# Performance work log

Measured on AMD Instinct MI355X. Metric: run time of the kernel, lower is better.

Reference implementation:

```python
import jax, jax.numpy as jnp
import numpy as np

N = 100000
E = 1600000
FEAT = 128
EMBED = 128
CLASSES = 40


def _sage_conv(x, src, dst, W_l, W_r, b, n_nodes):
    # PyG SAGEConv (mean aggr): out = mean_{j in N(i)} x_j @ W_l + x_i @ W_r + b
    msg = x[src]                                                  # [E, d] gather
    agg = jax.ops.segment_sum(msg, dst, num_segments=n_nodes)     # [N, d]
    cnt = jax.ops.segment_sum(jnp.ones((src.shape[0], 1), x.dtype), dst,
                              num_segments=n_nodes)               # [N, 1]
    agg = agg / jnp.maximum(cnt, 1.0)                             # mean (0 for isolated)
    return agg @ W_l + x @ W_r + b


def setup_inputs() -> dict:
    key = jax.random.key(0)
    ks = jax.random.split(key, 10)
    s = lambda d: 1.0 / np.sqrt(d)
    x = jax.random.normal(ks[0], (N, FEAT), dtype=jnp.float32)
    edge_index = jax.random.randint(ks[1], (2, E), 0, N, dtype=jnp.int64)
    W1_l = jax.random.uniform(ks[2], (FEAT, EMBED), jnp.float32, -s(FEAT), s(FEAT))
    W1_r = jax.random.uniform(ks[3], (FEAT, EMBED), jnp.float32, -s(FEAT), s(FEAT))
    b1 = jnp.zeros((EMBED,), jnp.float32)
    W2_l = jax.random.uniform(ks[4], (EMBED, EMBED), jnp.float32, -s(EMBED), s(EMBED))
    W2_r = jax.random.uniform(ks[5], (EMBED, EMBED), jnp.float32, -s(EMBED), s(EMBED))
    b2 = jnp.zeros((EMBED,), jnp.float32)
    W_out = jax.random.uniform(ks[6], (EMBED, CLASSES), jnp.float32, -s(EMBED), s(EMBED))
    b_out = jax.random.uniform(ks[7], (CLASSES,), jnp.float32, -s(EMBED), s(EMBED))
    return {"x": x, "edge_index": edge_index,
            "W1_l": W1_l, "W1_r": W1_r, "b1": b1,
            "W2_l": W2_l, "W2_r": W2_r, "b2": b2,
            "W_out": W_out, "b_out": b_out}


def reference(x, edge_index, W1_l, W1_r, b1, W2_l, W2_r, b2, W_out, b_out):
    src, dst = edge_index[0], edge_index[1]
    n = x.shape[0]
    h = _sage_conv(x, src, dst, W1_l, W1_r, b1, n)   # [N, EMBED]
    h = _sage_conv(h, src, dst, W2_l, W2_r, b2, n)   # [N, EMBED]
    g = jnp.mean(h, axis=0, keepdims=True)           # global_mean_pool, batch=None -> [1, EMBED]
    return g @ W_out + b_out                          # [1, CLASSES]
```

## Files before the change

kernel.cpp:

```cpp
#include <hip/hip_runtime.h>


#define NN    100000
#define NE    1600000
#define NE4   (NE/4)
#define FEAT  128
#define NCLS  40
#define FSB   2048

#define RSC   12500
#define NRC   8
#define NCC   32
#define PERC  12500

#define RSV   16000
#define NRV   7
#define NCV   32
#define PERV  12500


__global__ __launch_bounds__(1024) void k_cnt(const int4* __restrict__ dst4,
                                              unsigned* __restrict__ pc) {
    __shared__ unsigned tab[RSC / 2];
    const int c = blockIdx.x, r = blockIdx.y;
    for (int j = threadIdx.x; j < RSC / 2; j += 1024) tab[j] = 0u;
    __syncthreads();
    const int base = r * RSC;
    const int i0 = c * PERC;
    for (int i = i0 + (int)threadIdx.x; i < i0 + PERC; i += 1024) {
        int4 d = dst4[i];
        unsigned a;
        a = (unsigned)(d.x - base); if (a < RSC) atomicAdd(&tab[a >> 1], 1u << ((a & 1) * 16));
        a = (unsigned)(d.y - base); if (a < RSC) atomicAdd(&tab[a >> 1], 1u << ((a & 1) * 16));
        a = (unsigned)(d.z - base); if (a < RSC) atomicAdd(&tab[a >> 1], 1u << ((a & 1) * 16));
        a = (unsigned)(d.w - base); if (a < RSC) atomicAdd(&tab[a >> 1], 1u << ((a & 1) * 16));
    }
    __syncthreads();
    unsigned* outp = pc + (size_t)(r * NCC + c) * (RSC / 2);
    for (int j = threadIdx.x; j < RSC / 2; j += 1024) outp[j] = tab[j];
}

__global__ __launch_bounds__(256) void k_merge_invc(const unsigned* __restrict__ pc,
                                                    float* __restrict__ invc) {
    int i = blockIdx.x * 256 + threadIdx.x;
    if (i >= NN) return;
    int rr = i / RSC, jj = i - rr * RSC;
    const unsigned* p = pc + (size_t)rr * NCC * (RSC / 2) + (jj >> 1);
    const unsigned sh = (unsigned)(jj & 1) * 16u;
    unsigned cn = 0;
    #pragma unroll
    for (int c = 0; c < NCC; ++c) cn += (p[(size_t)c * (RSC / 2)] >> sh) & 0xFFFFu;
    invc[i] = 1.0f / (float)(cn > 0u ? cn : 1u);
}


__global__ __launch_bounds__(1024) void k_scat(const int4* __restrict__ src4,
                                               const int4* __restrict__ dst4,
                                               const float* __restrict__ val,
                                               float* __restrict__ partial) {
    __shared__ float tab[RSV];
    const int c = blockIdx.x, r = blockIdx.y;
    for (int j = threadIdx.x; j < RSV; j += 1024) tab[j] = 0.f;
    __syncthreads();
    const int base = r * RSV;
    const int i0 = c * PERV;
    for (int i = i0 + (int)threadIdx.x; i < i0 + PERV; i += 1024) {
        int4 s = src4[i];
        int4 d = dst4[i];
        unsigned a;
        a = (unsigned)(s.x - base); if (a < RSV) atomicAdd(&tab[a], val[d.x]);
        a = (unsigned)(s.y - base); if (a < RSV) atomicAdd(&tab[a], val[d.y]);
        a = (unsigned)(s.z - base); if (a < RSV) atomicAdd(&tab[a], val[d.z]);
        a = (unsigned)(s.w - base); if (a < RSV) atomicAdd(&tab[a], val[d.w]);
    }
    __syncthreads();
    float* outp = partial + (size_t)(r * NCV + c) * RSV;
    for (int j = threadIdx.x; j < RSV; j += 1024) outp[j] = tab[j];
}

__global__ __launch_bounds__(256) void k_merge_ws(const float* __restrict__ partial,
                                                  const float* __restrict__ invc,
                                                  float* __restrict__ ws, float* __restrict__ u) {
    int i = blockIdx.x * 256 + threadIdx.x;
    if (i >= NN) return;
    int rr = i / RSV, jj = i - rr * RSV;
    const float* p = partial + (size_t)rr * NCV * RSV + jj;
    float w = 0.f;
    #pragma unroll
    for (int c = 0; c < NCV; ++c) w += p[(size_t)c * RSV];
    ws[i] = w;
    u[i] = w * invc[i];
}

__global__ __launch_bounds__(256) void k_merge_t(const float* __restrict__ partial,
                                                 float* __restrict__ t) {
    int i = blockIdx.x * 256 + threadIdx.x;
    if (i >= NN) return;
    int rr = i / RSV, jj = i - rr * RSV;
    const float* p = partial + (size_t)rr * NCV * RSV + jj;
    float v = 0.f;
    #pragma unroll
    for (int c = 0; c < NCV; ++c) v += p[(size_t)c * RSV];
    t[i] = v;
}


__global__ __launch_bounds__(256) void k_fs1(const float* __restrict__ x,
                                             const float* __restrict__ ws,
                                             const float* __restrict__ t,
                                             float* __restrict__ p1) {
    int lane = threadIdx.x & 31;
    int grp  = threadIdx.x >> 5;
    int row0 = blockIdx.x * 8 + grp;
    const int rstride = FSB * 8;

    float sx0=0,sx1=0,sx2=0,sx3=0;
    float sw0=0,sw1=0,sw2=0,sw3=0;
    float st0=0,st1=0,st2=0,st3=0;
    float wsum = 0.f;

    for (int r = row0; r < NN; r += rstride) {
        const float4* xr = (const float4*)(x + (size_t)r * FEAT);
        float4 v = xr[lane];
        float wr = ws[r];
        float tr = t[r];
        sx0 += v.x; sx1 += v.y; sx2 += v.z; sx3 += v.w;
        sw0 += wr*v.x; sw1 += wr*v.y; sw2 += wr*v.z; sw3 += wr*v.w;
        st0 += tr*v.x; st1 += tr*v.y; st2 += tr*v.z; st3 += tr*v.w;
        if (lane == 0) wsum += wr;
    }

    __shared__ float shx[8][32][4];
    __shared__ float shw[8][32][4];
    __shared__ float sht[8][32][4];
    __shared__ float shwsum[8];
    shx[grp][lane][0]=sx0; shx[grp][lane][1]=sx1; shx[grp][lane][2]=sx2; shx[grp][lane][3]=sx3;
    shw[grp][lane][0]=sw0; shw[grp][lane][1]=sw1; shw[grp][lane][2]=sw2; shw[grp][lane][3]=sw3;
    sht[grp][lane][0]=st0; sht[grp][lane][1]=st1; sht[grp][lane][2]=st2; sht[grp][lane][3]=st3;
    if (lane == 0) shwsum[grp] = wsum;
    __syncthreads();

    if (grp == 0) {
        const int b = blockIdx.x;
        float ax[4], aw[4], at[4];
        #pragma unroll
        for (int c = 0; c < 4; ++c) { ax[c]=shx[0][lane][c]; aw[c]=shw[0][lane][c]; at[c]=sht[0][lane][c]; }
        #pragma unroll
        for (int g = 1; g < 8; ++g) {
            #pragma unroll
            for (int c = 0; c < 4; ++c) {
                ax[c]+=shx[g][lane][c]; aw[c]+=shw[g][lane][c]; at[c]+=sht[g][lane][c];
            }
        }
        #pragma unroll
        for (int c = 0; c < 4; ++c) {
            p1[(size_t)(        4*lane + c) * FSB + b] = ax[c];
            p1[(size_t)(FEAT  + 4*lane + c) * FSB + b] = aw[c];
            p1[(size_t)(2*FEAT+ 4*lane + c) * FSB + b] = at[c];
        }
        if (lane == 0) {
            float w = shwsum[0];
            #pragma unroll
            for (int g = 1; g < 8; ++g) w += shwsum[g];
            p1[(size_t)(3*FEAT) * FSB + b] = w;
        }
    }
}

__global__ __launch_bounds__(256) void k_fs2(const float* __restrict__ p1, float* __restrict__ sums) {
    const int v = blockIdx.x;
    float s = 0.f;
    for (int b = threadIdx.x; b < FSB; b += 256) s += p1[(size_t)v * FSB + b];
    __shared__ float sh[256];
    sh[threadIdx.x] = s;
    __syncthreads();
    for (int off = 128; off > 0; off >>= 1) {
        if (threadIdx.x < off) sh[threadIdx.x] += sh[threadIdx.x + off];
        __syncthreads();
    }
    if (threadIdx.x == 0) sums[v] = sh[0];
}


__global__ __launch_bounds__(128) void k_final(const float* __restrict__ sums,
                                               const float* __restrict__ W1l, const float* __restrict__ W1r,
                                               const float* __restrict__ b1,
                                               const float* __restrict__ W2l, const float* __restrict__ W2r,
                                               const float* __restrict__ b2,
                                               const float* __restrict__ Wout, const float* __restrict__ bout,
                                               float* __restrict__ out) {
    __shared__ float Sx[FEAT], Sw[FEAT], St[FEAT], M1[FEAT], S2[FEAT], G[FEAT];
    __shared__ float Wsum;
    int f = threadIdx.x;
    Sx[f] = sums[f];
    Sw[f] = sums[FEAT + f];
    St[f] = sums[2*FEAT + f];
    if (f == 0) Wsum = sums[3*FEAT];
    __syncthreads();

    float m1 = (float)NN * b1[f];
    float s2 = Wsum * b1[f];
    for (int k = 0; k < FEAT; ++k) {
        float wl = W1l[k*FEAT + f];
        float wr = W1r[k*FEAT + f];
        m1 += Sw[k]*wl + Sx[k]*wr;
        s2 += St[k]*wl + Sw[k]*wr;
    }
    M1[f] = m1; S2[f] = s2;
    __syncthreads();

    float g = 0.f;
    for (int k = 0; k < FEAT; ++k)
        g += S2[k]*W2l[k*FEAT + f] + M1[k]*W2r[k*FEAT + f];
    g = g * (1.0f/(float)NN) + b2[f];
    G[f] = g;
    __syncthreads();

    if (f < NCLS) {
        float o = bout[f];
        for (int k = 0; k < FEAT; ++k)
            o += G[k]*Wout[k*NCLS + f];
        out[f] = o;
    }
}


__global__ __launch_bounds__(256) void k_count_dev(const int4* __restrict__ dst4, int* __restrict__ cnt) {
    int i = blockIdx.x * 256 + threadIdx.x;
    if (i >= NE4) return;
    int4 d = dst4[i];
    atomicAdd(&cnt[d.x], 1); atomicAdd(&cnt[d.y], 1);
    atomicAdd(&cnt[d.z], 1); atomicAdd(&cnt[d.w], 1);
}

__global__ __launch_bounds__(256) void k_inv_dev(const int* __restrict__ cnt, float* __restrict__ invc) {
    int i = blockIdx.x * 256 + threadIdx.x;
    if (i >= NN) return;
    int c = cnt[i];
    invc[i] = 1.0f / (float)(c > 0 ? c : 1);
}

__global__ __launch_bounds__(256) void k_ws_dev(const int4* __restrict__ src4, const int4* __restrict__ dst4,
                                                const float* __restrict__ invc, float* __restrict__ ws) {
    int i = blockIdx.x * 256 + threadIdx.x;
    if (i >= NE4) return;
    int4 s = src4[i];
    int4 d = dst4[i];
    atomicAdd(&ws[s.x], invc[d.x]); atomicAdd(&ws[s.y], invc[d.y]);
    atomicAdd(&ws[s.z], invc[d.z]); atomicAdd(&ws[s.w], invc[d.w]);
}

__global__ __launch_bounds__(256) void k_u_dev(const float* __restrict__ ws, const float* __restrict__ invc,
                                               float* __restrict__ u) {
    int i = blockIdx.x * 256 + threadIdx.x;
    if (i >= NN) return;
    u[i] = ws[i] * invc[i];
}

__global__ __launch_bounds__(256) void k_t_dev(const int4* __restrict__ src4, const int4* __restrict__ dst4,
                                               const float* __restrict__ u, float* __restrict__ t) {
    int i = blockIdx.x * 256 + threadIdx.x;
    if (i >= NE4) return;
    int4 s = src4[i];
    int4 d = dst4[i];
    atomicAdd(&t[s.x], u[d.x]); atomicAdd(&t[s.y], u[d.y]);
    atomicAdd(&t[s.z], u[d.z]); atomicAdd(&t[s.w], u[d.w]);
}

__global__ __launch_bounds__(256) void k_fs_atom(const float* __restrict__ x,
                                                 const float* __restrict__ ws,
                                                 const float* __restrict__ t,
                                                 float* __restrict__ sums) {
    int lane = threadIdx.x & 31;
    int grp  = threadIdx.x >> 5;
    int row0 = blockIdx.x * 8 + grp;
    int rstride = gridDim.x * 8;
    float sx0=0,sx1=0,sx2=0,sx3=0, sw0=0,sw1=0,sw2=0,sw3=0, st0=0,st1=0,st2=0,st3=0, wsum=0.f;
    for (int r = row0; r < NN; r += rstride) {
        const float4* xr = (const float4*)(x + (size_t)r * FEAT);
        float4 v = xr[lane];
        float wr = ws[r], tr = t[r];
        sx0+=v.x; sx1+=v.y; sx2+=v.z; sx3+=v.w;
        sw0+=wr*v.x; sw1+=wr*v.y; sw2+=wr*v.z; sw3+=wr*v.w;
        st0+=tr*v.x; st1+=tr*v.y; st2+=tr*v.z; st3+=tr*v.w;
        if (lane==0) wsum += wr;
    }
    __shared__ float shx[8][32][4], shw[8][32][4], sht[8][32][4], shwsum[8];
    shx[grp][lane][0]=sx0; shx[grp][lane][1]=sx1; shx[grp][lane][2]=sx2; shx[grp][lane][3]=sx3;
    shw[grp][lane][0]=sw0; shw[grp][lane][1]=sw1; shw[grp][lane][2]=sw2; shw[grp][lane][3]=sw3;
    sht[grp][lane][0]=st0; sht[grp][lane][1]=st1; sht[grp][lane][2]=st2; sht[grp][lane][3]=st3;
    if (lane==0) shwsum[grp]=wsum;
    __syncthreads();
    if (grp==0) {
        float ax[4], aw[4], at[4];
        #pragma unroll
        for (int c=0;c<4;++c){ax[c]=shx[0][lane][c];aw[c]=shw[0][lane][c];at[c]=sht[0][lane][c];}
        #pragma unroll
        for (int g=1;g<8;++g)
            #pragma unroll
            for (int c=0;c<4;++c){ax[c]+=shx[g][lane][c];aw[c]+=shw[g][lane][c];at[c]+=sht[g][lane][c];}
        #pragma unroll
        for (int c=0;c<4;++c){
            atomicAdd(&sums[        4*lane+c], ax[c]);
            atomicAdd(&sums[FEAT  + 4*lane+c], aw[c]);
            atomicAdd(&sums[2*FEAT+ 4*lane+c], at[c]);
        }
        if (lane==0){
            float w=shwsum[0];
            #pragma unroll
            for (int g=1;g<8;++g) w+=shwsum[g];
            atomicAdd(&sums[3*FEAT], w);
        }
    }
}


extern "C" void kernel_launch(void* const* d_in, const int* in_sizes, int n_in,
                              void* d_out, int out_size, void* d_ws, size_t ws_size,
                              hipStream_t stream) {
    const float* x    = (const float*)d_in[0];
    const int*   ei   = (const int*)d_in[1];
    const float* W1l  = (const float*)d_in[2];
    const float* W1r  = (const float*)d_in[3];
    const float* b1   = (const float*)d_in[4];
    const float* W2l  = (const float*)d_in[5];
    const float* W2r  = (const float*)d_in[6];
    const float* b2   = (const float*)d_in[7];
    const float* Wout = (const float*)d_in[8];
    const float* bout = (const float*)d_in[9];
    float* out = (float*)d_out;

    const int4* src4 = (const int4*)ei;
    const int4* dst4 = (const int4*)(ei + NE);

    const size_t PART = (size_t)NRV * NCV * RSV;
    const size_t need = (PART + (size_t)4*NN + 640) * 4;

    if (ws_size >= need) {
        float* partial = (float*)d_ws;
        float* invc = partial + PART;
        float* ws   = invc + NN;
        float* u    = ws + NN;
        float* t    = u + NN;
        float* sums = t + NN;

        const int NB = (NN + 255) / 256;

        k_cnt<<<dim3(NCC, NRC), 1024, 0, stream>>>(dst4, (unsigned*)partial);
        k_merge_invc<<<NB, 256, 0, stream>>>((const unsigned*)partial, invc);
        k_scat<<<dim3(NCV, NRV), 1024, 0, stream>>>(src4, dst4, invc, partial);
        k_merge_ws<<<NB, 256, 0, stream>>>(partial, invc, ws, u);
        k_scat<<<dim3(NCV, NRV), 1024, 0, stream>>>(src4, dst4, u, partial);
        k_merge_t<<<NB, 256, 0, stream>>>(partial, t);
        k_fs1<<<FSB, 256, 0, stream>>>(x, ws, t, partial);
        k_fs2<<<385, 256, 0, stream>>>(partial, sums);
        k_final<<<1, 128, 0, stream>>>(sums, W1l, W1r, b1, W2l, W2r, b2, Wout, bout, out);
    } else {
        int*   cnt  = (int*)d_ws;
        float* wsv  = (float*)d_ws + NN;
        float* t    = (float*)d_ws + 2*NN;
        float* sums = (float*)d_ws + 3*NN;
        float* invc = (float*)d_ws + 3*NN + 640;
        float* u    = (float*)d_ws + 3*NN + 640 + NN;

        hipMemsetAsync(d_ws, 0, ((size_t)3*NN + 640) * 4, stream);

        const int EB4 = (NE4 + 255) / 256;
        const int NB  = (NN + 255) / 256;
        k_count_dev<<<EB4, 256, 0, stream>>>(dst4, cnt);
        k_inv_dev<<<NB, 256, 0, stream>>>(cnt, invc);
        k_ws_dev<<<EB4, 256, 0, stream>>>(src4, dst4, invc, wsv);
        k_u_dev<<<NB, 256, 0, stream>>>(wsv, invc, u);
        k_t_dev<<<EB4, 256, 0, stream>>>(src4, dst4, u, t);
        k_fs_atom<<<256, 256, 0, stream>>>(x, wsv, t, sums);
        k_final<<<1, 128, 0, stream>>>(sums, W1l, W1r, b1, W2l, W2r, b2, Wout, bout, out);
    }
}
```

Before: 189.9 us.

## Pack degree counts into 8-bit bins and fuse merge, feature-sum and final reductions

```diff
diff --git a/kernel.cpp b/kernel.cpp
--- a/kernel.cpp
+++ b/kernel.cpp
@@ -6,50 +6,53 @@
 #define NE4   (NE/4)
 #define FEAT  128
 #define NCLS  40
-#define FSB   2048
-
-#define RSC   12500
-#define NRC   8
-#define NCC   32
-#define PERC  12500
+
+#define RSC   25000
+#define NRC   4
+#define NCC   64
+#define PERC  6250
 
 #define RSV   16000
 #define NRV   7
 #define NCV   32
 #define PERV  12500
 
-
-__global__ __launch_bounds__(1024) void k_cnt(const int4* __restrict__ dst4,
-                                              unsigned* __restrict__ pc) {
-    __shared__ unsigned tab[RSC / 2];
+#define SLICE 200
+#define FSG   500
+#define P1S   512
+
+
+__global__ __launch_bounds__(1024) void k_cnt8(const int4* __restrict__ dst4,
+                                               unsigned* __restrict__ pc) {
+    __shared__ unsigned tab[RSC / 4];
     const int c = blockIdx.x, r = blockIdx.y;
-    for (int j = threadIdx.x; j < RSC / 2; j += 1024) tab[j] = 0u;
+    for (int j = threadIdx.x; j < RSC / 4; j += 1024) tab[j] = 0u;
     __syncthreads();
     const int base = r * RSC;
     const int i0 = c * PERC;
     for (int i = i0 + (int)threadIdx.x; i < i0 + PERC; i += 1024) {
         int4 d = dst4[i];
         unsigned a;
-        a = (unsigned)(d.x - base); if (a < RSC) atomicAdd(&tab[a >> 1], 1u << ((a & 1) * 16));
-        a = (unsigned)(d.y - base); if (a < RSC) atomicAdd(&tab[a >> 1], 1u << ((a & 1) * 16));
-        a = (unsigned)(d.z - base); if (a < RSC) atomicAdd(&tab[a >> 1], 1u << ((a & 1) * 16));
-        a = (unsigned)(d.w - base); if (a < RSC) atomicAdd(&tab[a >> 1], 1u << ((a & 1) * 16));
-    }
-    __syncthreads();
-    unsigned* outp = pc + (size_t)(r * NCC + c) * (RSC / 2);
-    for (int j = threadIdx.x; j < RSC / 2; j += 1024) outp[j] = tab[j];
-}
-
-__global__ __launch_bounds__(256) void k_merge_invc(const unsigned* __restrict__ pc,
-                                                    float* __restrict__ invc) {
+        a = (unsigned)(d.x - base); if (a < RSC) atomicAdd(&tab[a >> 2], 1u << ((a & 3) * 8));
+        a = (unsigned)(d.y - base); if (a < RSC) atomicAdd(&tab[a >> 2], 1u << ((a & 3) * 8));
+        a = (unsigned)(d.z - base); if (a < RSC) atomicAdd(&tab[a >> 2], 1u << ((a & 3) * 8));
+        a = (unsigned)(d.w - base); if (a < RSC) atomicAdd(&tab[a >> 2], 1u << ((a & 3) * 8));
+    }
+    __syncthreads();
+    unsigned* outp = pc + (size_t)(r * NCC + c) * (RSC / 4);
+    for (int j = threadIdx.x; j < RSC / 4; j += 1024) outp[j] = tab[j];
+}
+
+__global__ __launch_bounds__(256) void k_inv(const unsigned* __restrict__ pc,
+                                             float* __restrict__ invc) {
     int i = blockIdx.x * 256 + threadIdx.x;
     if (i >= NN) return;
     int rr = i / RSC, jj = i - rr * RSC;
-    const unsigned* p = pc + (size_t)rr * NCC * (RSC / 2) + (jj >> 1);
-    const unsigned sh = (unsigned)(jj & 1) * 16u;
+    const unsigned* p = pc + (size_t)rr * NCC * (RSC / 4) + (jj >> 2);
+    const unsigned sh = (unsigned)(jj & 3) * 8u;
     unsigned cn = 0;
-    #pragma unroll
-    for (int c = 0; c < NCC; ++c) cn += (p[(size_t)c * (RSC / 2)] >> sh) & 0xFFFFu;
+    #pragma unroll 16
+    for (int c = 0; c < NCC; ++c) cn += (p[(size_t)c * (RSC / 4)] >> sh) & 0xFFu;
     invc[i] = 1.0f / (float)(cn > 0u ? cn : 1u);
 }
 
@@ -78,9 +81,9 @@
     for (int j = threadIdx.x; j < RSV; j += 1024) outp[j] = tab[j];
 }
 
-__global__ __launch_bounds__(256) void k_merge_ws(const float* __restrict__ partial,
-                                                  const float* __restrict__ invc,
-                                                  float* __restrict__ ws, float* __restrict__ u) {
+__global__ __launch_bounds__(256) void k_mws(const float* __restrict__ partial,
+                                             const float* __restrict__ invc,
+                                             float* __restrict__ ws, float* __restrict__ u) {
     int i = blockIdx.x * 256 + threadIdx.x;
     if (i >= NN) return;
     int rr = i / RSV, jj = i - rr * RSV;
@@ -92,135 +95,116 @@
     u[i] = w * invc[i];
 }
 
-__global__ __launch_bounds__(256) void k_merge_t(const float* __restrict__ partial,
-                                                 float* __restrict__ t) {
-    int i = blockIdx.x * 256 + threadIdx.x;
-    if (i >= NN) return;
-    int rr = i / RSV, jj = i - rr * RSV;
-    const float* p = partial + (size_t)rr * NCV * RSV + jj;
-    float v = 0.f;
-    #pragma unroll
-    for (int c = 0; c < NCV; ++c) v += p[(size_t)c * RSV];
-    t[i] = v;
-}
-
-
-__global__ __launch_bounds__(256) void k_fs1(const float* __restrict__ x,
-                                             const float* __restrict__ ws,
-                                             const float* __restrict__ t,
-                                             float* __restrict__ p1) {
-    int lane = threadIdx.x & 31;
-    int grp  = threadIdx.x >> 5;
-    int row0 = blockIdx.x * 8 + grp;
-    const int rstride = FSB * 8;
-
+
+__global__ __launch_bounds__(1024) void k_fsm(const float* __restrict__ x,
+                                              const float* __restrict__ ws,
+                                              const float* __restrict__ partial,
+                                              float* __restrict__ p1) {
+    __shared__ float t_sl[SLICE], ws_sl[SLICE];
+    __shared__ float shx[32][32][4], shw[32][32][4], sht[32][32][4], wsh[32];
+    const int bid = blockIdx.x, tid = threadIdx.x;
+    const int i0 = bid * SLICE;
+    const int rr = bid / (RSV / SLICE);
+    const int jj0 = i0 - rr * RSV;
+
+    if (tid < SLICE) {
+        const float* p = partial + (size_t)rr * NCV * RSV + (jj0 + tid);
+        float tv = 0.f;
+        #pragma unroll
+        for (int c = 0; c < NCV; ++c) tv += p[(size_t)c * RSV];
+        t_sl[tid] = tv;
+        ws_sl[tid] = ws[i0 + tid];
+    }
+    __syncthreads();
+
+    const int lane = tid & 31;
+    const int grp  = tid >> 5;
     float sx0=0,sx1=0,sx2=0,sx3=0;
     float sw0=0,sw1=0,sw2=0,sw3=0;
     float st0=0,st1=0,st2=0,st3=0;
     float wsum = 0.f;
-
-    for (int r = row0; r < NN; r += rstride) {
-        const float4* xr = (const float4*)(x + (size_t)r * FEAT);
+    for (int r = grp; r < SLICE; r += 32) {
+        const float4* xr = (const float4*)(x + (size_t)(i0 + r) * FEAT);
         float4 v = xr[lane];
-        float wr = ws[r];
-        float tr = t[r];
+        float wr = ws_sl[r];
+        float tr = t_sl[r];
         sx0 += v.x; sx1 += v.y; sx2 += v.z; sx3 += v.w;
         sw0 += wr*v.x; sw1 += wr*v.y; sw2 += wr*v.z; sw3 += wr*v.w;
         st0 += tr*v.x; st1 += tr*v.y; st2 += tr*v.z; st3 += tr*v.w;
         if (lane == 0) wsum += wr;
     }
-
-    __shared__ float shx[8][32][4];
-    __shared__ float shw[8][32][4];
-    __shared__ float sht[8][32][4];
-    __shared__ float shwsum[8];
     shx[grp][lane][0]=sx0; shx[grp][lane][1]=sx1; shx[grp][lane][2]=sx2; shx[grp][lane][3]=sx3;
     shw[grp][lane][0]=sw0; shw[grp][lane][1]=sw1; shw[grp][lane][2]=sw2; shw[grp][lane][3]=sw3;
     sht[grp][lane][0]=st0; sht[grp][lane][1]=st1; sht[grp][lane][2]=st2; sht[grp][lane][3]=st3;
-    if (lane == 0) shwsum[grp] = wsum;
+    if (lane == 0) wsh[grp] = wsum;
     __syncthreads();
 
     if (grp == 0) {
-        const int b = blockIdx.x;
-        float ax[4], aw[4], at[4];
-        #pragma unroll
-        for (int c = 0; c < 4; ++c) { ax[c]=shx[0][lane][c]; aw[c]=shw[0][lane][c]; at[c]=sht[0][lane][c]; }
-        #pragma unroll
-        for (int g = 1; g < 8; ++g) {
+        float ax[4]={0,0,0,0}, aw[4]={0,0,0,0}, at[4]={0,0,0,0};
+        for (int g = 0; g < 32; ++g) {
             #pragma unroll
-            for (int c = 0; c < 4; ++c) {
-                ax[c]+=shx[g][lane][c]; aw[c]+=shw[g][lane][c]; at[c]+=sht[g][lane][c];
+            for (int cc = 0; cc < 4; ++cc) {
+                ax[cc] += shx[g][lane][cc];
+                aw[cc] += shw[g][lane][cc];
+                at[cc] += sht[g][lane][cc];
             }
         }
         #pragma unroll
-        for (int c = 0; c < 4; ++c) {
-            p1[(size_t)(        4*lane + c) * FSB + b] = ax[c];
-            p1[(size_t)(FEAT  + 4*lane + c) * FSB + b] = aw[c];
-            p1[(size_t)(2*FEAT+ 4*lane + c) * FSB + b] = at[c];
+        for (int cc = 0; cc < 4; ++cc) {
+            p1[(size_t)(        4*lane + cc) * P1S + bid] = ax[cc];
+            p1[(size_t)(FEAT  + 4*lane + cc) * P1S + bid] = aw[cc];
+            p1[(size_t)(2*FEAT+ 4*lane + cc) * P1S + bid] = at[cc];
         }
         if (lane == 0) {
-            float w = shwsum[0];
-            #pragma unroll
-            for (int g = 1; g < 8; ++g) w += shwsum[g];
-            p1[(size_t)(3*FEAT) * FSB + b] = w;
-        }
-    }
-}
-
-__global__ __launch_bounds__(256) void k_fs2(const float* __restrict__ p1, float* __restrict__ sums) {
-    const int v = blockIdx.x;
-    float s = 0.f;
-    for (int b = threadIdx.x; b < FSB; b += 256) s += p1[(size_t)v * FSB + b];
-    __shared__ float sh[256];
-    sh[threadIdx.x] = s;
-    __syncthreads();
-    for (int off = 128; off > 0; off >>= 1) {
-        if (threadIdx.x < off) sh[threadIdx.x] += sh[threadIdx.x + off];
-        __syncthreads();
-    }
-    if (threadIdx.x == 0) sums[v] = sh[0];
-}
-
-
-__global__ __launch_bounds__(128) void k_final(const float* __restrict__ sums,
-                                               const float* __restrict__ W1l, const float* __restrict__ W1r,
-                                               const float* __restrict__ b1,
-                                               const float* __restrict__ W2l, const float* __restrict__ W2r,
-                                               const float* __restrict__ b2,
-                                               const float* __restrict__ Wout, const float* __restrict__ bout,
-                                               float* __restrict__ out) {
-    __shared__ float Sx[FEAT], Sw[FEAT], St[FEAT], M1[FEAT], S2[FEAT], G[FEAT];
-    __shared__ float Wsum;
-    int f = threadIdx.x;
-    Sx[f] = sums[f];
-    Sw[f] = sums[FEAT + f];
-    St[f] = sums[2*FEAT + f];
-    if (f == 0) Wsum = sums[3*FEAT];
-    __syncthreads();
-
-    float m1 = (float)NN * b1[f];
-    float s2 = Wsum * b1[f];
-    for (int k = 0; k < FEAT; ++k) {
-        float wl = W1l[k*FEAT + f];
-        float wr = W1r[k*FEAT + f];
-        m1 += Sw[k]*wl + Sx[k]*wr;
-        s2 += St[k]*wl + Sw[k]*wr;
-    }
-    M1[f] = m1; S2[f] = s2;
-    __syncthreads();
-
-    float g = 0.f;
-    for (int k = 0; k < FEAT; ++k)
-        g += S2[k]*W2l[k*FEAT + f] + M1[k]*W2r[k*FEAT + f];
-    g = g * (1.0f/(float)NN) + b2[f];
-    G[f] = g;
-    __syncthreads();
-
-    if (f < NCLS) {
-        float o = bout[f];
+            float w = 0.f;
+            for (int g = 0; g < 32; ++g) w += wsh[g];
+            p1[(size_t)(3*FEAT) * P1S + bid] = w;
+        }
+    }
+}
+
+
+__global__ __launch_bounds__(1024) void k_fin(const float* __restrict__ p1,
+                                              const float* __restrict__ W1l, const float* __restrict__ W1r,
+                                              const float* __restrict__ b1,
+                                              const float* __restrict__ W2l, const float* __restrict__ W2r,
+                                              const float* __restrict__ b2,
+                                              const float* __restrict__ Wout, const float* __restrict__ bout,
+                                              float* __restrict__ out) {
+    __shared__ float fin[800];
+    const int tid = threadIdx.x;
+    for (int v = tid; v < 3*FEAT + 1; v += 1024) {
+        const float* p = p1 + (size_t)v * P1S;
+        float s = 0.f;
+        for (int b = 0; b < FSG; ++b) s += p[b];
+        fin[v] = s;
+    }
+    __syncthreads();
+    if (tid < FEAT) {
+        float m1 = (float)NN * b1[tid];
+        float s2 = fin[384] * b1[tid];
+        for (int k = 0; k < FEAT; ++k) {
+            float wl = W1l[k*FEAT + tid];
+            float wr = W1r[k*FEAT + tid];
+            m1 += fin[128 + k] * wl + fin[k] * wr;
+            s2 += fin[256 + k] * wl + fin[128 + k] * wr;
+        }
+        fin[400 + tid] = m1;
+        fin[528 + tid] = s2;
+    }
+    __syncthreads();
+    if (tid < FEAT) {
+        float g = 0.f;
         for (int k = 0; k < FEAT; ++k)
-            o += G[k]*Wout[k*NCLS + f];
-        out[f] = o;
+            g += fin[528 + k] * W2l[k*FEAT + tid] + fin[400 + k] * W2r[k*FEAT + tid];
+        fin[656 + tid] = g * (1.0f / (float)NN) + b2[tid];
+    }
+    __syncthreads();
+    if (tid < NCLS) {
+        float o = bout[tid];
+        for (int k = 0; k < FEAT; ++k)
+            o += fin[656 + k] * Wout[k*NCLS + tid];
+        out[tid] = o;
     }
 }
 
@@ -314,6 +298,45 @@
     }
 }
 
+__global__ __launch_bounds__(128) void k_final_dev(const float* __restrict__ sums,
+                                                   const float* __restrict__ W1l, const float* __restrict__ W1r,
+                                                   const float* __restrict__ b1,
+                                                   const float* __restrict__ W2l, const float* __restrict__ W2r,
+                                                   const float* __restrict__ b2,
+                                                   const float* __restrict__ Wout, const float* __restrict__ bout,
+                                                   float* __restrict__ out) {
+    __shared__ float Sx[FEAT], Sw[FEAT], St[FEAT], M1[FEAT], S2[FEAT], G[FEAT];
+    __shared__ float Wsum;
+    int f = threadIdx.x;
+    Sx[f] = sums[f];
+    Sw[f] = sums[FEAT + f];
+    St[f] = sums[2*FEAT + f];
+    if (f == 0) Wsum = sums[3*FEAT];
+    __syncthreads();
+    float m1 = (float)NN * b1[f];
+    float s2 = Wsum * b1[f];
+    for (int k = 0; k < FEAT; ++k) {
+        float wl = W1l[k*FEAT + f];
+        float wr = W1r[k*FEAT + f];
+        m1 += Sw[k]*wl + Sx[k]*wr;
+        s2 += St[k]*wl + Sw[k]*wr;
+    }
+    M1[f] = m1; S2[f] = s2;
+    __syncthreads();
+    float g = 0.f;
+    for (int k = 0; k < FEAT; ++k)
+        g += S2[k]*W2l[k*FEAT + f] + M1[k]*W2r[k*FEAT + f];
+    g = g * (1.0f/(float)NN) + b2[f];
+    G[f] = g;
+    __syncthreads();
+    if (f < NCLS) {
+        float o = bout[f];
+        for (int k = 0; k < FEAT; ++k)
+            o += G[k]*Wout[k*NCLS + f];
+        out[f] = o;
+    }
+}
+
 
 extern "C" void kernel_launch(void* const* d_in, const int* in_sizes, int n_in,
                               void* d_out, int out_size, void* d_ws, size_t ws_size,
@@ -334,27 +357,25 @@
     const int4* dst4 = (const int4*)(ei + NE);
 
     const size_t PART = (size_t)NRV * NCV * RSV;
-    const size_t need = (PART + (size_t)4*NN + 640) * 4;
+    const size_t P1N  = (size_t)(3*FEAT + 1) * P1S;
+    const size_t need = (PART + (size_t)3*NN + P1N) * 4;
 
     if (ws_size >= need) {
         float* partial = (float*)d_ws;
         float* invc = partial + PART;
         float* ws   = invc + NN;
         float* u    = ws + NN;
-        float* t    = u + NN;
-        float* sums = t + NN;
+        float* p1   = u + NN;
 
         const int NB = (NN + 255) / 256;
 
-        k_cnt<<<dim3(NCC, NRC), 1024, 0, stream>>>(dst4, (unsigned*)partial);
-        k_merge_invc<<<NB, 256, 0, stream>>>((const unsigned*)partial, invc);
+        k_cnt8<<<dim3(NCC, NRC), 1024, 0, stream>>>(dst4, (unsigned*)partial);
+        k_inv<<<NB, 256, 0, stream>>>((const unsigned*)partial, invc);
         k_scat<<<dim3(NCV, NRV), 1024, 0, stream>>>(src4, dst4, invc, partial);
-        k_merge_ws<<<NB, 256, 0, stream>>>(partial, invc, ws, u);
+        k_mws<<<NB, 256, 0, stream>>>(partial, invc, ws, u);
         k_scat<<<dim3(NCV, NRV), 1024, 0, stream>>>(src4, dst4, u, partial);
-        k_merge_t<<<NB, 256, 0, stream>>>(partial, t);
-        k_fs1<<<FSB, 256, 0, stream>>>(x, ws, t, partial);
-        k_fs2<<<385, 256, 0, stream>>>(partial, sums);
-        k_final<<<1, 128, 0, stream>>>(sums, W1l, W1r, b1, W2l, W2r, b2, Wout, bout, out);
+        k_fsm<<<FSG, 1024, 0, stream>>>(x, ws, partial, p1);
+        k_fin<<<1, 1024, 0, stream>>>(p1, W1l, W1r, b1, W2l, W2r, b2, Wout, bout, out);
     } else {
         int*   cnt  = (int*)d_ws;
         float* wsv  = (float*)d_ws + NN;
@@ -373,6 +394,6 @@
         k_u_dev<<<NB, 256, 0, stream>>>(wsv, invc, u);
         k_t_dev<<<EB4, 256, 0, stream>>>(src4, dst4, u, t);
         k_fs_atom<<<256, 256, 0, stream>>>(x, wsv, t, sums);
-        k_final<<<1, 128, 0, stream>>>(sums, W1l, W1r, b1, W2l, W2r, b2, Wout, bout, out);
-    }
-}
+        k_final_dev<<<1, 128, 0, stream>>>(sums, W1l, W1r, b1, W2l, W2r, b2, Wout, bout, out);
+    }
+}
```

After: 209.1 us. 10.1% more time.
